# Kernel optimization log

Hardware: AMD Instinct MI355X
Metric: run time of the kernel (lower is better)

## Reference

```python
import jax, jax.numpy as jnp
import numpy as np
from functools import partial

# ---- constants mirroring init_kwargs ----
T, B, J, I = 1024, 32, 128, 512
KD = 16              # max_delay (dilated kernel size)
THETA = 1.0          # threshold
SIG = 0.5            # delay.SIG, frozen (requires_grad=False)
ALPHA = 5.0          # ATan surrogate alpha
EPS = 1e-5           # BatchNorm eps

# ---- ATan surrogate spike (spikingjelly): fwd = heaviside, bwd = atan grad ----
@jax.custom_vjp
def atan_spike(x):
    return (x >= 0).astype(x.dtype)

def _atan_fwd(x):
    return atan_spike(x), x

def _atan_bwd(x, g):
    return (g * (ALPHA / 2.0) / (1.0 + (jnp.pi / 2.0 * ALPHA * x) ** 2),)

atan_spike.defvjp(_atan_fwd, _atan_bwd)

def _dcls_kernel(w, P):
    # DCLS1d 'gauss' version, kernel_count=1: gaussian bump centered at P + KD//2,
    # normalized over the kernel axis, scaled by weight. w,P: (I,J) -> (I,J,KD)
    c = P + KD // 2
    k = jnp.arange(KD, dtype=w.dtype)                        # (KD,)
    g = jnp.exp(-0.5 * ((k[None, None, :] - c[:, :, None]) / SIG) ** 2)
    g = g / (g.sum(-1, keepdims=True) + 1e-7)
    return w[:, :, None] * g                                  # (I,J,KD)

def setup_inputs() -> dict:
    key = jax.random.key(0)
    ks = jax.random.split(key, 6)
    x = jax.random.normal(ks[0], (T, B, J), dtype=jnp.float32)
    # kaiming_uniform_ fan_in = J*1 -> bound = sqrt(6/fan_in)
    bound = float(np.sqrt(6.0 / J))
    delay_w = jax.random.uniform(ks[1], (I, J), jnp.float32, -bound, bound)
    # P ~ U(-max_delay//2, max_delay//2), then clamped (already in range)
    delay_P = jax.random.uniform(ks[2], (I, J), jnp.float32, -(KD // 2), KD // 2)
    beta = jax.random.uniform(ks[3], (I,), jnp.float32, 0.0, 1.0)
    bn_gamma = jnp.ones((I,), jnp.float32)
    bn_beta = jnp.zeros((I,), jnp.float32)
    U0 = jax.random.uniform(ks[4], (B, I), jnp.float32)       # RandomBatchwiseInit(0,1)
    return {"x": x, "delay_w": delay_w, "delay_P": delay_P, "beta": beta,
            "bn_gamma": bn_gamma, "bn_beta": bn_beta, "U0": U0}

def reference(x, delay_w, delay_P, beta, bn_gamma, bn_beta, U0):
    # --- delayed conv: (T,B,J) -> (B,J,T) -> left-pad KD-1 -> conv1d -> (T,B,I) ---
    xb = jnp.transpose(x, (1, 2, 0))                          # (B,J,T)
    xb = jnp.pad(xb, ((0, 0), (0, 0), (KD - 1, 0)))           # (B,J,T+KD-1)
    kern = _dcls_kernel(delay_w, delay_P)                     # (I,J,KD)
    y = jax.lax.conv_general_dilated(
        xb, kern, window_strides=(1,), padding='VALID',
        dimension_numbers=('NCH', 'OIH', 'NCH'))              # (B,I,T)
    y = jnp.transpose(y, (2, 0, 1))                           # (T,B,I)

    # --- BatchNorm1d over reshaped (T*B, I, 1): stats over T*B per channel ---
    yf = y.reshape(T * B, I)
    mean = yf.mean(axis=0)
    var = yf.var(axis=0)
    yf = (yf - mean) * jax.lax.rsqrt(var + EPS) * bn_gamma + bn_beta
    y = yf.reshape(T, B, I)

    # --- soft-reset LIF scan (NOTE: original passes RAW beta, not sigmoid(beta)) ---
    def step(carry, xt):
        Ut, St = carry
        Ut = beta * (Ut - THETA * St) + (1.0 - beta) * xt
        St = atan_spike(Ut - THETA)
        return (Ut, St), St

    S0 = jnp.zeros_like(U0)
    _, o = jax.lax.scan(step, (U0, S0), y)                    # (T,B,I)
    return o
```

## Files before the change

kernel.cpp:

```cpp
#include <hip/hip_runtime.h>

#define TT 1024
#define NB 32
#define NJ 128
#define NI 512
#define KD 16
#define LDP 40

typedef short bf16x8 __attribute__((ext_vector_type(8)));
typedef short bf16x4 __attribute__((ext_vector_type(4)));
typedef float floatx4 __attribute__((ext_vector_type(4)));

struct S3 { short h, m, l; };

__device__ __forceinline__ S3 split3(float v) {
    S3 o;
    unsigned hb = __float_as_uint(v) & 0xFFFF0000u;
    float hf = __uint_as_float(hb);
    float r1 = v - hf;
    unsigned mb = __float_as_uint(r1) & 0xFFFF0000u;
    float mf = __uint_as_float(mb);
    float r2 = r1 - mf;
    unsigned lb = __float_as_uint(r2) & 0xFFFF0000u;
    o.h = (short)(hb >> 16);
    o.m = (short)(mb >> 16);
    o.l = (short)(lb >> 16);
    return o;
}

__global__ __launch_bounds__(256) void dcls_kern(const float* __restrict__ w,
                                                 const float* __restrict__ P,
                                                 float* __restrict__ Wt) {
    int idx = blockIdx.x * 256 + threadIdx.x;
    int j = idx & (NJ - 1);
    int i = idx >> 7;
    float wv = w[i * NJ + j];
    float c  = P[i * NJ + j] + (float)(KD / 2);
    float g[KD];
    float s = 0.f;
#pragma unroll
    for (int k = 0; k < KD; ++k) {
        float u = (float)k - c;
        g[k] = expf(-2.0f * u * u);
        s += g[k];
    }
    float inv = wv / (s + 1e-7f);
#pragma unroll
    for (int k = 0; k < KD; ++k) {
        int d = (KD - 1) - k;
        Wt[(size_t)i * 2048 + d * NJ + j] = g[k] * inv;
    }
}

__global__ __launch_bounds__(256) void conv_mfma(const float* __restrict__ x,
                                                 const float* __restrict__ Wt,
                                                 float* __restrict__ y) {
    __shared__ short Ah[128][LDP];
    __shared__ short Am[128][LDP];
    __shared__ short Al[128][LDP];
    __shared__ short Wh[128][LDP];
    __shared__ short Wm[128][LDP];
    __shared__ short Wl[128][LDP];

    const int t0 = blockIdx.x * 128;
    const int i0 = blockIdx.y * 128;
    const int b  = blockIdx.z;
    const int tid = threadIdx.x;

    const int lane8 = tid & 7;
    const int rw    = tid >> 3;
    const int l    = tid & 63;
    const int wid  = tid >> 6;
    const int lr16 = l & 15;
    const int kb   = l >> 4;
    const int wm   = wid >> 1;
    const int wn   = wid & 1;

    floatx4 acc[4][4];
#pragma unroll
    for (int mf = 0; mf < 4; ++mf)
#pragma unroll
        for (int nf = 0; nf < 4; ++nf)
#pragma unroll
            for (int e = 0; e < 4; ++e) acc[mf][nf][e] = 0.f;

#pragma unroll 1
    for (int kk = 0; kk < 64; ++kk) {
        const int d   = kk >> 2;
        const int j0c = (kk & 3) << 5;

        float4 ga[4], gw[4];
#pragma unroll
        for (int s = 0; s < 4; ++s) {
            int r = rw + s * 32;
            int t = t0 + r - d;
            float4 va = make_float4(0.f, 0.f, 0.f, 0.f);
            if (t >= 0) va = *(const float4*)(x + ((size_t)t * NB + b) * NJ + j0c + lane8 * 4);
            ga[s] = va;
            gw[s] = *(const float4*)(Wt + (size_t)(i0 + r) * 2048 + kk * 32 + lane8 * 4);
        }

        __syncthreads();

#pragma unroll
        for (int s = 0; s < 4; ++s) {
            int r  = rw + s * 32;
            int c4 = lane8 * 4;
            S3 s0 = split3(ga[s].x), s1 = split3(ga[s].y), s2 = split3(ga[s].z), s3 = split3(ga[s].w);
            bf16x4 h4, m4, l4;
            h4[0] = s0.h; m4[0] = s0.m; l4[0] = s0.l;
            h4[1] = s1.h; m4[1] = s1.m; l4[1] = s1.l;
            h4[2] = s2.h; m4[2] = s2.m; l4[2] = s2.l;
            h4[3] = s3.h; m4[3] = s3.m; l4[3] = s3.l;
            *(bf16x4*)&Ah[r][c4] = h4;
            *(bf16x4*)&Am[r][c4] = m4;
            *(bf16x4*)&Al[r][c4] = l4;
            s0 = split3(gw[s].x); s1 = split3(gw[s].y); s2 = split3(gw[s].z); s3 = split3(gw[s].w);
            h4[0] = s0.h; m4[0] = s0.m; l4[0] = s0.l;
            h4[1] = s1.h; m4[1] = s1.m; l4[1] = s1.l;
            h4[2] = s2.h; m4[2] = s2.m; l4[2] = s2.l;
            h4[3] = s3.h; m4[3] = s3.m; l4[3] = s3.l;
            *(bf16x4*)&Wh[r][c4] = h4;
            *(bf16x4*)&Wm[r][c4] = m4;
            *(bf16x4*)&Wl[r][c4] = l4;
        }

        __syncthreads();

        bf16x8 bh[4], bm[4], bl2[4];
#pragma unroll
        for (int nf = 0; nf < 4; ++nf) {
            int row = wn * 64 + nf * 16 + lr16;
            bh[nf]  = *(const bf16x8*)&Wh[row][kb * 8];
            bm[nf]  = *(const bf16x8*)&Wm[row][kb * 8];
            bl2[nf] = *(const bf16x8*)&Wl[row][kb * 8];
        }
#pragma unroll
        for (int mf = 0; mf < 4; ++mf) {
            int row = wm * 64 + mf * 16 + lr16;
            bf16x8 ah = *(const bf16x8*)&Ah[row][kb * 8];
            bf16x8 am = *(const bf16x8*)&Am[row][kb * 8];
            bf16x8 al = *(const bf16x8*)&Al[row][kb * 8];
#pragma unroll
            for (int nf = 0; nf < 4; ++nf)
                acc[mf][nf] = __builtin_amdgcn_mfma_f32_16x16x32_bf16(ah, bh[nf], acc[mf][nf], 0, 0, 0);
#pragma unroll
            for (int nf = 0; nf < 4; ++nf)
                acc[mf][nf] = __builtin_amdgcn_mfma_f32_16x16x32_bf16(ah, bm[nf], acc[mf][nf], 0, 0, 0);
#pragma unroll
            for (int nf = 0; nf < 4; ++nf)
                acc[mf][nf] = __builtin_amdgcn_mfma_f32_16x16x32_bf16(am, bh[nf], acc[mf][nf], 0, 0, 0);
#pragma unroll
            for (int nf = 0; nf < 4; ++nf)
                acc[mf][nf] = __builtin_amdgcn_mfma_f32_16x16x32_bf16(am, bm[nf], acc[mf][nf], 0, 0, 0);
#pragma unroll
            for (int nf = 0; nf < 4; ++nf)
                acc[mf][nf] = __builtin_amdgcn_mfma_f32_16x16x32_bf16(ah, bl2[nf], acc[mf][nf], 0, 0, 0);
#pragma unroll
            for (int nf = 0; nf < 4; ++nf)
                acc[mf][nf] = __builtin_amdgcn_mfma_f32_16x16x32_bf16(al, bh[nf], acc[mf][nf], 0, 0, 0);
        }
    }

#pragma unroll
    for (int mf = 0; mf < 4; ++mf)
#pragma unroll
        for (int nf = 0; nf < 4; ++nf) {
            int ic = i0 + wn * 64 + nf * 16 + lr16;
#pragma unroll
            for (int q = 0; q < 4; ++q) {
                int t = t0 + wm * 64 + mf * 16 + kb * 4 + q;
                y[((size_t)t * NB + b) * NI + ic] = acc[mf][nf][q];
            }
        }
}

__global__ __launch_bounds__(256) void red1(const float* __restrict__ y,
                                            float* __restrict__ part) {
    int r0 = blockIdx.x * 128;
    int c  = threadIdx.x;
    float s0 = 0.f, q0 = 0.f, s1 = 0.f, q1 = 0.f;
#pragma unroll 4
    for (int r = 0; r < 128; ++r) {
        float v0 = y[(size_t)(r0 + r) * NI + c];
        float v1 = y[(size_t)(r0 + r) * NI + c + 256];
        s0 += v0; q0 = fmaf(v0, v0, q0);
        s1 += v1; q1 = fmaf(v1, v1, q1);
    }
    part[blockIdx.x * NI + c]            = s0;
    part[blockIdx.x * NI + c + 256]      = s1;
    part[256 * NI + blockIdx.x * NI + c]       = q0;
    part[256 * NI + blockIdx.x * NI + c + 256] = q1;
}

__global__ __launch_bounds__(512) void red2(const float* __restrict__ part,
                                            const float* __restrict__ gamma,
                                            const float* __restrict__ bbeta,
                                            float* __restrict__ sb) {
    int c = threadIdx.x;
    double s = 0.0, q = 0.0;
#pragma unroll 8
    for (int p = 0; p < 256; ++p) {
        s += (double)part[p * NI + c];
        q += (double)part[256 * NI + p * NI + c];
    }
    double mean = s / 32768.0;
    double var  = q / 32768.0 - mean * mean;
    double scale = (double)gamma[c] / sqrt(var + 1e-5);
    sb[c]      = (float)scale;
    sb[NI + c] = (float)((double)bbeta[c] - mean * scale);
}

__global__ __launch_bounds__(64) void scan_kern(float* __restrict__ y,
                                                const float* __restrict__ sb,
                                                const float* __restrict__ beta,
                                                const float* __restrict__ U0) {
    int g = blockIdx.x * 64 + threadIdx.x;
    int i = g & (NI - 1);
    float scale = sb[i];
    float bias  = sb[NI + i];
    float bet = beta[i];
    float omb = 1.f - bet;
    float u = U0[g];
    float s = 0.f;
    float* yp = y + g;

    float A[32], Bv[32];
#pragma unroll
    for (int r = 0; r < 32; ++r) A[r] = yp[(size_t)r * 16384];

    for (int t0 = 0; t0 < TT; t0 += 64) {
#pragma unroll
        for (int r = 0; r < 32; ++r) Bv[r] = yp[(size_t)(t0 + 32 + r) * 16384];
#pragma unroll
        for (int r = 0; r < 32; ++r) {
            float z = fmaf(A[r], scale, bias);
            u = fmaf(bet, u - s, omb * z);
            s = (u >= 1.f) ? 1.f : 0.f;
            yp[(size_t)(t0 + r) * 16384] = s;
        }
        if (t0 + 64 < TT) {
#pragma unroll
            for (int r = 0; r < 32; ++r) A[r] = yp[(size_t)(t0 + 64 + r) * 16384];
        }
#pragma unroll
        for (int r = 0; r < 32; ++r) {
            float z = fmaf(Bv[r], scale, bias);
            u = fmaf(bet, u - s, omb * z);
            s = (u >= 1.f) ? 1.f : 0.f;
            yp[(size_t)(t0 + 32 + r) * 16384] = s;
        }
    }
}

extern "C" void kernel_launch(void* const* d_in, const int* in_sizes, int n_in,
                              void* d_out, int out_size, void* d_ws, size_t ws_size,
                              hipStream_t stream) {
    const float* x       = (const float*)d_in[0];
    const float* delay_w = (const float*)d_in[1];
    const float* delay_P = (const float*)d_in[2];
    const float* beta    = (const float*)d_in[3];
    const float* bn_g    = (const float*)d_in[4];
    const float* bn_b    = (const float*)d_in[5];
    const float* U0      = (const float*)d_in[6];
    float* y = (float*)d_out;

    float* Wt   = (float*)d_ws;
    float* part = Wt + (size_t)NI * 2048;
    float* sb   = part + 2 * 256 * NI;

    dcls_kern<<<dim3(NI * NJ / 256), dim3(256), 0, stream>>>(delay_w, delay_P, Wt);
    conv_mfma<<<dim3(TT / 128, NI / 128, NB), dim3(256), 0, stream>>>(x, Wt, y);
    red1<<<dim3(TT * NB / 128), dim3(256), 0, stream>>>(y, part);
    red2<<<dim3(1), dim3(512), 0, stream>>>(part, bn_g, bn_b, sb);
    scan_kern<<<dim3(NB * NI / 64), dim3(64), 0, stream>>>(y, sb, beta, U0);
}
```

Baseline: 413.3 us.

## Prefetch next K-slice into registers and XOR-swizzle packed LDS tiles

Moves the global loads for the next K iteration after the second barrier, so they overlap with the MFMA work of the current iteration. Packs the hi/mid/lo bf16 splits into three 128x64 shared arrays, each row XOR-swizzled at 16-byte granularity, replacing the padded layout. Each thread now stores one 16-byte vector per split piece instead of 8-byte ones. Adds launch_bounds occupancy 3, which raises register pressure from holding the prefetched data across the MFMA section.

```diff
diff --git a/kernel.cpp b/kernel.cpp
--- a/kernel.cpp
+++ b/kernel.cpp
@@ -5,10 +5,8 @@
 #define NJ 128
 #define NI 512
 #define KD 16
-#define LDP 40
 
 typedef short bf16x8 __attribute__((ext_vector_type(8)));
-typedef short bf16x4 __attribute__((ext_vector_type(4)));
 typedef float floatx4 __attribute__((ext_vector_type(4)));
 
 struct S3 { short h, m, l; };
@@ -52,23 +50,20 @@
     }
 }
 
-__global__ __launch_bounds__(256) void conv_mfma(const float* __restrict__ x,
-                                                 const float* __restrict__ Wt,
-                                                 float* __restrict__ y) {
-    __shared__ short Ah[128][LDP];
-    __shared__ short Am[128][LDP];
-    __shared__ short Al[128][LDP];
-    __shared__ short Wh[128][LDP];
-    __shared__ short Wm[128][LDP];
-    __shared__ short Wl[128][LDP];
+__global__ __launch_bounds__(256, 3) void conv_mfma(const float* __restrict__ x,
+                                                    const float* __restrict__ Wt,
+                                                    float* __restrict__ y) {
+    __shared__ __align__(16) short PA[128][64];
+    __shared__ __align__(16) short PW[128][64];
+    __shared__ __align__(16) short PL[128][64];
 
     const int t0 = blockIdx.x * 128;
     const int i0 = blockIdx.y * 128;
     const int b  = blockIdx.z;
     const int tid = threadIdx.x;
 
-    const int lane8 = tid & 7;
-    const int rw    = tid >> 3;
+    const int ch   = tid & 3;
+    const int rw2  = tid >> 2;
     const int l    = tid & 63;
     const int wid  = tid >> 6;
     const int lr16 = l & 15;
@@ -84,63 +79,98 @@
 #pragma unroll
             for (int e = 0; e < 4; ++e) acc[mf][nf][e] = 0.f;
 
+    float4 ga[2][2], gw[2][2];
+#pragma unroll
+    for (int s = 0; s < 2; ++s) {
+        int r = rw2 + s * 64;
+        int t = t0 + r;
+        const float* ax = x + ((size_t)t * NB + b) * NJ + ch * 8;
+        ga[s][0] = *(const float4*)ax;
+        ga[s][1] = *(const float4*)(ax + 4);
+        const float* wp = Wt + (size_t)(i0 + r) * 2048 + ch * 8;
+        gw[s][0] = *(const float4*)wp;
+        gw[s][1] = *(const float4*)(wp + 4);
+    }
+
 #pragma unroll 1
     for (int kk = 0; kk < 64; ++kk) {
-        const int d   = kk >> 2;
-        const int j0c = (kk & 3) << 5;
-
-        float4 ga[4], gw[4];
-#pragma unroll
-        for (int s = 0; s < 4; ++s) {
-            int r = rw + s * 32;
-            int t = t0 + r - d;
-            float4 va = make_float4(0.f, 0.f, 0.f, 0.f);
-            if (t >= 0) va = *(const float4*)(x + ((size_t)t * NB + b) * NJ + j0c + lane8 * 4);
-            ga[s] = va;
-            gw[s] = *(const float4*)(Wt + (size_t)(i0 + r) * 2048 + kk * 32 + lane8 * 4);
-        }
-
         __syncthreads();
 
 #pragma unroll
-        for (int s = 0; s < 4; ++s) {
-            int r  = rw + s * 32;
-            int c4 = lane8 * 4;
-            S3 s0 = split3(ga[s].x), s1 = split3(ga[s].y), s2 = split3(ga[s].z), s3 = split3(ga[s].w);
-            bf16x4 h4, m4, l4;
-            h4[0] = s0.h; m4[0] = s0.m; l4[0] = s0.l;
-            h4[1] = s1.h; m4[1] = s1.m; l4[1] = s1.l;
-            h4[2] = s2.h; m4[2] = s2.m; l4[2] = s2.l;
-            h4[3] = s3.h; m4[3] = s3.m; l4[3] = s3.l;
-            *(bf16x4*)&Ah[r][c4] = h4;
-            *(bf16x4*)&Am[r][c4] = m4;
-            *(bf16x4*)&Al[r][c4] = l4;
-            s0 = split3(gw[s].x); s1 = split3(gw[s].y); s2 = split3(gw[s].z); s3 = split3(gw[s].w);
-            h4[0] = s0.h; m4[0] = s0.m; l4[0] = s0.l;
-            h4[1] = s1.h; m4[1] = s1.m; l4[1] = s1.l;
-            h4[2] = s2.h; m4[2] = s2.m; l4[2] = s2.l;
-            h4[3] = s3.h; m4[3] = s3.m; l4[3] = s3.l;
-            *(bf16x4*)&Wh[r][c4] = h4;
-            *(bf16x4*)&Wm[r][c4] = m4;
-            *(bf16x4*)&Wl[r][c4] = l4;
+        for (int s = 0; s < 2; ++s) {
+            int r   = rw2 + s * 64;
+            int key = r & 7;
+            char* rowA = (char*)PA + r * 128;
+            char* rowW = (char*)PW + r * 128;
+            char* rowL = (char*)PL + r * 128;
+            bf16x8 h8, m8, l8;
+#pragma unroll
+            for (int q = 0; q < 2; ++q) {
+                float4 v = ga[s][q];
+                S3 a = split3(v.x), bb = split3(v.y), cc = split3(v.z), dd = split3(v.w);
+                h8[q*4+0] = a.h;  h8[q*4+1] = bb.h; h8[q*4+2] = cc.h; h8[q*4+3] = dd.h;
+                m8[q*4+0] = a.m;  m8[q*4+1] = bb.m; m8[q*4+2] = cc.m; m8[q*4+3] = dd.m;
+                l8[q*4+0] = a.l;  l8[q*4+1] = bb.l; l8[q*4+2] = cc.l; l8[q*4+3] = dd.l;
+            }
+            *(bf16x8*)(rowA + ((ch     ^ key) * 16)) = h8;
+            *(bf16x8*)(rowA + (((ch+4) ^ key) * 16)) = m8;
+            *(bf16x8*)(rowL + ((ch     ^ key) * 16)) = l8;
+#pragma unroll
+            for (int q = 0; q < 2; ++q) {
+                float4 v = gw[s][q];
+                S3 a = split3(v.x), bb = split3(v.y), cc = split3(v.z), dd = split3(v.w);
+                h8[q*4+0] = a.h;  h8[q*4+1] = bb.h; h8[q*4+2] = cc.h; h8[q*4+3] = dd.h;
+                m8[q*4+0] = a.m;  m8[q*4+1] = bb.m; m8[q*4+2] = cc.m; m8[q*4+3] = dd.m;
+                l8[q*4+0] = a.l;  l8[q*4+1] = bb.l; l8[q*4+2] = cc.l; l8[q*4+3] = dd.l;
+            }
+            *(bf16x8*)(rowW + ((ch     ^ key) * 16)) = h8;
+            *(bf16x8*)(rowW + (((ch+4) ^ key) * 16)) = m8;
+            *(bf16x8*)(rowL + (((ch+4) ^ key) * 16)) = l8;
         }
 
         __syncthreads();
+
+        if (kk + 1 < 64) {
+            const int kn  = kk + 1;
+            const int d   = kn >> 2;
+            const int j0c = (kn & 3) << 5;
+#pragma unroll
+            for (int s = 0; s < 2; ++s) {
+                int r = rw2 + s * 64;
+                int t = t0 + r - d;
+                float4 z = make_float4(0.f, 0.f, 0.f, 0.f);
+                ga[s][0] = z; ga[s][1] = z;
+                if (t >= 0) {
+                    const float* ax = x + ((size_t)t * NB + b) * NJ + j0c + ch * 8;
+                    ga[s][0] = *(const float4*)ax;
+                    ga[s][1] = *(const float4*)(ax + 4);
+                }
+                const float* wp = Wt + (size_t)(i0 + r) * 2048 + kn * 32 + ch * 8;
+                gw[s][0] = *(const float4*)wp;
+                gw[s][1] = *(const float4*)(wp + 4);
+            }
+        }
 
         bf16x8 bh[4], bm[4], bl2[4];
 #pragma unroll
         for (int nf = 0; nf < 4; ++nf) {
             int row = wn * 64 + nf * 16 + lr16;
-            bh[nf]  = *(const bf16x8*)&Wh[row][kb * 8];
-            bm[nf]  = *(const bf16x8*)&Wm[row][kb * 8];
-            bl2[nf] = *(const bf16x8*)&Wl[row][kb * 8];
+            int key = row & 7;
+            const char* rowW = (const char*)PW + row * 128;
+            const char* rowL = (const char*)PL + row * 128;
+            bh[nf]  = *(const bf16x8*)(rowW + ((kb     ^ key) * 16));
+            bm[nf]  = *(const bf16x8*)(rowW + (((kb+4) ^ key) * 16));
+            bl2[nf] = *(const bf16x8*)(rowL + (((kb+4) ^ key) * 16));
         }
 #pragma unroll
         for (int mf = 0; mf < 4; ++mf) {
             int row = wm * 64 + mf * 16 + lr16;
-            bf16x8 ah = *(const bf16x8*)&Ah[row][kb * 8];
-            bf16x8 am = *(const bf16x8*)&Am[row][kb * 8];
-            bf16x8 al = *(const bf16x8*)&Al[row][kb * 8];
+            int key = row & 7;
+            const char* rowA = (const char*)PA + row * 128;
+            const char* rowL = (const char*)PL + row * 128;
+            bf16x8 ah = *(const bf16x8*)(rowA + ((kb     ^ key) * 16));
+            bf16x8 am = *(const bf16x8*)(rowA + (((kb+4) ^ key) * 16));
+            bf16x8 al = *(const bf16x8*)(rowL + ((kb     ^ key) * 16));
 #pragma unroll
             for (int nf = 0; nf < 4; ++nf)
                 acc[mf][nf] = __builtin_amdgcn_mfma_f32_16x16x32_bf16(ah, bh[nf], acc[mf][nf], 0, 0, 0);
```

New measurement: 436.2 us. +5.5%, slower.

## Pre-split weights into MFMA fragment layout and read them directly from global

Applied to the files above, without the earlier changes.

The DCLS kernel now writes the weights already split into three bf16 levels and stored in MFMA fragment order, so the conv kernel loads B fragments straight from global memory instead of staging them through shared memory and splitting them on every tile. The A tile is packed into swizzled shared memory (hi and mid in one array, lo in another) to avoid bank conflicts. The next step's x and weights are prefetched into registers while the current step runs its MFMAs, and launch bounds ask for two blocks per CU. This saves shared-memory traffic and repeated split work, at the cost of more register pressure and workspace aliasing: WF and the reduction partials share the same workspace region, which is safe only because the conv kernel finishes before red1 starts.

```diff
diff --git a/kernel.cpp b/kernel.cpp
--- a/kernel.cpp
+++ b/kernel.cpp
@@ -5,10 +5,9 @@
 #define NJ 128
 #define NI 512
 #define KD 16
-#define LDP 40
+#define LVL 1048576
 
 typedef short bf16x8 __attribute__((ext_vector_type(8)));
-typedef short bf16x4 __attribute__((ext_vector_type(4)));
 typedef float floatx4 __attribute__((ext_vector_type(4)));
 
 struct S3 { short h, m, l; };
@@ -30,7 +29,7 @@
 
 __global__ __launch_bounds__(256) void dcls_kern(const float* __restrict__ w,
                                                  const float* __restrict__ P,
-                                                 float* __restrict__ Wt) {
+                                                 short* __restrict__ WF) {
     int idx = blockIdx.x * 256 + threadIdx.x;
     int j = idx & (NJ - 1);
     int i = idx >> 7;
@@ -45,30 +44,30 @@
         s += g[k];
     }
     float inv = wv / (s + 1e-7f);
-#pragma unroll
-    for (int k = 0; k < KD; ++k) {
-        int d = (KD - 1) - k;
-        Wt[(size_t)i * 2048 + d * NJ + j] = g[k] * inv;
-    }
-}
-
-__global__ __launch_bounds__(256) void conv_mfma(const float* __restrict__ x,
-                                                 const float* __restrict__ Wt,
-                                                 float* __restrict__ y) {
-    __shared__ short Ah[128][LDP];
-    __shared__ short Am[128][LDP];
-    __shared__ short Al[128][LDP];
-    __shared__ short Wh[128][LDP];
-    __shared__ short Wm[128][LDP];
-    __shared__ short Wl[128][LDP];
+    size_t base = (size_t)(i >> 4) * 32768 + (size_t)(j >> 3) * 128 + (i & 15) * 8 + (j & 7);
+#pragma unroll
+    for (int d = 0; d < KD; ++d) {
+        S3 sp = split3(g[(KD - 1) - d] * inv);
+        size_t off = base + (size_t)d * 2048;
+        WF[off]           = sp.h;
+        WF[off + LVL]     = sp.m;
+        WF[off + 2 * LVL] = sp.l;
+    }
+}
+
+__global__ __launch_bounds__(256, 2) void conv_mfma(const float* __restrict__ x,
+                                                    const short* __restrict__ WF,
+                                                    float* __restrict__ y) {
+    __shared__ __align__(16) short PA[128][64];
+    __shared__ __align__(16) short PL[128][64];
 
     const int t0 = blockIdx.x * 128;
     const int i0 = blockIdx.y * 128;
     const int b  = blockIdx.z;
     const int tid = threadIdx.x;
 
-    const int lane8 = tid & 7;
-    const int rw    = tid >> 3;
+    const int ch   = tid & 3;
+    const int rw2  = tid >> 2;
     const int l    = tid & 63;
     const int wid  = tid >> 6;
     const int lr16 = l & 15;
@@ -76,6 +75,13 @@
     const int wm   = wid >> 1;
     const int wn   = wid & 1;
 
+    const short* pnf[4];
+#pragma unroll
+    for (int nf = 0; nf < 4; ++nf) {
+        int ig = (i0 + wn * 64 + nf * 16) >> 4;
+        pnf[nf] = WF + (size_t)ig * 32768 + l * 8;
+    }
+
     floatx4 acc[4][4];
 #pragma unroll
     for (int mf = 0; mf < 4; ++mf)
@@ -84,83 +90,90 @@
 #pragma unroll
             for (int e = 0; e < 4; ++e) acc[mf][nf][e] = 0.f;
 
+    float4 ga[2][2];
+    bf16x8 W0h[4], W0m[4], W0l[4], W1h[4], W1m[4], W1l[4];
+
+#define LOADW(K, H, M, L_) {                                                    \
+    int koff = ((((K) >> 2) * 16 + ((K) & 3) * 4)) * 128;                       \
+    _Pragma("unroll") for (int nf = 0; nf < 4; ++nf) {                          \
+        const short* p = pnf[nf] + koff;                                        \
+        H[nf]  = *(const bf16x8*)(p);                                           \
+        M[nf]  = *(const bf16x8*)(p + LVL);                                     \
+        L_[nf] = *(const bf16x8*)(p + 2 * LVL); } }
+
+#define STEP(K, CH, CM, CL, NH, NM, NL) {                                       \
+    __syncthreads();                                                            \
+    _Pragma("unroll") for (int s = 0; s < 2; ++s) {                             \
+        int r = rw2 + s * 64;                                                   \
+        int key = r & 7;                                                        \
+        char* rowA = (char*)PA + r * 128;                                       \
+        char* rowL = (char*)PL + r * 128;                                       \
+        S3 a0 = split3(ga[s][0].x), a1 = split3(ga[s][0].y),                    \
+           a2 = split3(ga[s][0].z), a3 = split3(ga[s][0].w),                    \
+           a4 = split3(ga[s][1].x), a5 = split3(ga[s][1].y),                    \
+           a6 = split3(ga[s][1].z), a7 = split3(ga[s][1].w);                    \
+        bf16x8 h8, m8, l8;                                                      \
+        h8[0]=a0.h; h8[1]=a1.h; h8[2]=a2.h; h8[3]=a3.h;                         \
+        h8[4]=a4.h; h8[5]=a5.h; h8[6]=a6.h; h8[7]=a7.h;                         \
+        m8[0]=a0.m; m8[1]=a1.m; m8[2]=a2.m; m8[3]=a3.m;                         \
+        m8[4]=a4.m; m8[5]=a5.m; m8[6]=a6.m; m8[7]=a7.m;                         \
+        l8[0]=a0.l; l8[1]=a1.l; l8[2]=a2.l; l8[3]=a3.l;                         \
+        l8[4]=a4.l; l8[5]=a5.l; l8[6]=a6.l; l8[7]=a7.l;                         \
+        *(bf16x8*)(rowA + ((ch ^ key) * 16))       = h8;                        \
+        *(bf16x8*)(rowA + (((ch + 4) ^ key) * 16)) = m8;                        \
+        *(bf16x8*)(rowL + ((ch ^ key) * 16))       = l8; }                      \
+    __syncthreads();                                                            \
+    if ((K) + 1 < 64) {                                                         \
+        int kn = (K) + 1, dn = kn >> 2, j0n = (kn & 3) << 5;                    \
+        _Pragma("unroll") for (int s = 0; s < 2; ++s) {                         \
+            int r = rw2 + s * 64;                                               \
+            int t = t0 + r - dn;                                                \
+            float4 z4 = make_float4(0.f, 0.f, 0.f, 0.f);                        \
+            ga[s][0] = z4; ga[s][1] = z4;                                       \
+            if (t >= 0) {                                                       \
+                const float* ax = x + ((size_t)t * NB + b) * NJ + j0n + ch * 8; \
+                ga[s][0] = *(const float4*)ax;                                  \
+                ga[s][1] = *(const float4*)(ax + 4); } }                        \
+        LOADW(kn, NH, NM, NL) }                                                 \
+    _Pragma("unroll") for (int mf = 0; mf < 4; ++mf) {                          \
+        int row = wm * 64 + mf * 16 + lr16;                                     \
+        int key = row & 7;                                                      \
+        const char* rowA = (const char*)PA + row * 128;                         \
+        const char* rowL = (const char*)PL + row * 128;                         \
+        bf16x8 ah = *(const bf16x8*)(rowA + ((kb ^ key) * 16));                 \
+        bf16x8 am = *(const bf16x8*)(rowA + (((kb + 4) ^ key) * 16));           \
+        bf16x8 al = *(const bf16x8*)(rowL + ((kb ^ key) * 16));                 \
+        _Pragma("unroll") for (int nf = 0; nf < 4; ++nf)                        \
+            acc[mf][nf] = __builtin_amdgcn_mfma_f32_16x16x32_bf16(ah, CH[nf], acc[mf][nf], 0, 0, 0); \
+        _Pragma("unroll") for (int nf = 0; nf < 4; ++nf)                        \
+            acc[mf][nf] = __builtin_amdgcn_mfma_f32_16x16x32_bf16(ah, CM[nf], acc[mf][nf], 0, 0, 0); \
+        _Pragma("unroll") for (int nf = 0; nf < 4; ++nf)                        \
+            acc[mf][nf] = __builtin_amdgcn_mfma_f32_16x16x32_bf16(am, CH[nf], acc[mf][nf], 0, 0, 0); \
+        _Pragma("unroll") for (int nf = 0; nf < 4; ++nf)                        \
+            acc[mf][nf] = __builtin_amdgcn_mfma_f32_16x16x32_bf16(am, CM[nf], acc[mf][nf], 0, 0, 0); \
+        _Pragma("unroll") for (int nf = 0; nf < 4; ++nf)                        \
+            acc[mf][nf] = __builtin_amdgcn_mfma_f32_16x16x32_bf16(ah, CL[nf], acc[mf][nf], 0, 0, 0); \
+        _Pragma("unroll") for (int nf = 0; nf < 4; ++nf)                        \
+            acc[mf][nf] = __builtin_amdgcn_mfma_f32_16x16x32_bf16(al, CH[nf], acc[mf][nf], 0, 0, 0); \
+    } }
+
+#pragma unroll
+    for (int s = 0; s < 2; ++s) {
+        int r = rw2 + s * 64;
+        int t = t0 + r;
+        const float* ax = x + ((size_t)t * NB + b) * NJ + ch * 8;
+        ga[s][0] = *(const float4*)ax;
+        ga[s][1] = *(const float4*)(ax + 4);
+    }
+    LOADW(0, W0h, W0m, W0l)
+
 #pragma unroll 1
-    for (int kk = 0; kk < 64; ++kk) {
-        const int d   = kk >> 2;
-        const int j0c = (kk & 3) << 5;
-
-        float4 ga[4], gw[4];
-#pragma unroll
-        for (int s = 0; s < 4; ++s) {
-            int r = rw + s * 32;
-            int t = t0 + r - d;
-            float4 va = make_float4(0.f, 0.f, 0.f, 0.f);
-            if (t >= 0) va = *(const float4*)(x + ((size_t)t * NB + b) * NJ + j0c + lane8 * 4);
-            ga[s] = va;
-            gw[s] = *(const float4*)(Wt + (size_t)(i0 + r) * 2048 + kk * 32 + lane8 * 4);
-        }
-
-        __syncthreads();
-
-#pragma unroll
-        for (int s = 0; s < 4; ++s) {
-            int r  = rw + s * 32;
-            int c4 = lane8 * 4;
-            S3 s0 = split3(ga[s].x), s1 = split3(ga[s].y), s2 = split3(ga[s].z), s3 = split3(ga[s].w);
-            bf16x4 h4, m4, l4;
-            h4[0] = s0.h; m4[0] = s0.m; l4[0] = s0.l;
-            h4[1] = s1.h; m4[1] = s1.m; l4[1] = s1.l;
-            h4[2] = s2.h; m4[2] = s2.m; l4[2] = s2.l;
-            h4[3] = s3.h; m4[3] = s3.m; l4[3] = s3.l;
-            *(bf16x4*)&Ah[r][c4] = h4;
-            *(bf16x4*)&Am[r][c4] = m4;
-            *(bf16x4*)&Al[r][c4] = l4;
-            s0 = split3(gw[s].x); s1 = split3(gw[s].y); s2 = split3(gw[s].z); s3 = split3(gw[s].w);
-            h4[0] = s0.h; m4[0] = s0.m; l4[0] = s0.l;
-            h4[1] = s1.h; m4[1] = s1.m; l4[1] = s1.l;
-            h4[2] = s2.h; m4[2] = s2.m; l4[2] = s2.l;
-            h4[3] = s3.h; m4[3] = s3.m; l4[3] = s3.l;
-            *(bf16x4*)&Wh[r][c4] = h4;
-            *(bf16x4*)&Wm[r][c4] = m4;
-            *(bf16x4*)&Wl[r][c4] = l4;
-        }
-
-        __syncthreads();
-
-        bf16x8 bh[4], bm[4], bl2[4];
-#pragma unroll
-        for (int nf = 0; nf < 4; ++nf) {
-            int row = wn * 64 + nf * 16 + lr16;
-            bh[nf]  = *(const bf16x8*)&Wh[row][kb * 8];
-            bm[nf]  = *(const bf16x8*)&Wm[row][kb * 8];
-            bl2[nf] = *(const bf16x8*)&Wl[row][kb * 8];
-        }
-#pragma unroll
-        for (int mf = 0; mf < 4; ++mf) {
-            int row = wm * 64 + mf * 16 + lr16;
-            bf16x8 ah = *(const bf16x8*)&Ah[row][kb * 8];
-            bf16x8 am = *(const bf16x8*)&Am[row][kb * 8];
-            bf16x8 al = *(const bf16x8*)&Al[row][kb * 8];
-#pragma unroll
-            for (int nf = 0; nf < 4; ++nf)
-                acc[mf][nf] = __builtin_amdgcn_mfma_f32_16x16x32_bf16(ah, bh[nf], acc[mf][nf], 0, 0, 0);
-#pragma unroll
-            for (int nf = 0; nf < 4; ++nf)
-                acc[mf][nf] = __builtin_amdgcn_mfma_f32_16x16x32_bf16(ah, bm[nf], acc[mf][nf], 0, 0, 0);
-#pragma unroll
-            for (int nf = 0; nf < 4; ++nf)
-                acc[mf][nf] = __builtin_amdgcn_mfma_f32_16x16x32_bf16(am, bh[nf], acc[mf][nf], 0, 0, 0);
-#pragma unroll
-            for (int nf = 0; nf < 4; ++nf)
-                acc[mf][nf] = __builtin_amdgcn_mfma_f32_16x16x32_bf16(am, bm[nf], acc[mf][nf], 0, 0, 0);
-#pragma unroll
-            for (int nf = 0; nf < 4; ++nf)
-                acc[mf][nf] = __builtin_amdgcn_mfma_f32_16x16x32_bf16(ah, bl2[nf], acc[mf][nf], 0, 0, 0);
-#pragma unroll
-            for (int nf = 0; nf < 4; ++nf)
-                acc[mf][nf] = __builtin_amdgcn_mfma_f32_16x16x32_bf16(al, bh[nf], acc[mf][nf], 0, 0, 0);
-        }
-    }
+    for (int kk = 0; kk < 64; kk += 2) {
+        STEP(kk,     W0h, W0m, W0l, W1h, W1m, W1l)
+        STEP(kk + 1, W1h, W1m, W1l, W0h, W0m, W0l)
+    }
+#undef LOADW
+#undef STEP
 
 #pragma unroll
     for (int mf = 0; mf < 4; ++mf)
@@ -265,12 +278,12 @@
     const float* U0      = (const float*)d_in[6];
     float* y = (float*)d_out;
 
-    float* Wt   = (float*)d_ws;
-    float* part = Wt + (size_t)NI * 2048;
-    float* sb   = part + 2 * 256 * NI;
-
-    dcls_kern<<<dim3(NI * NJ / 256), dim3(256), 0, stream>>>(delay_w, delay_P, Wt);
-    conv_mfma<<<dim3(TT / 128, NI / 128, NB), dim3(256), 0, stream>>>(x, Wt, y);
+    short* WF   = (short*)d_ws;
+    float* part = (float*)d_ws;
+    float* sb   = (float*)d_ws + 2 * 256 * NI;
+
+    dcls_kern<<<dim3(NI * NJ / 256), dim3(256), 0, stream>>>(delay_w, delay_P, WF);
+    conv_mfma<<<dim3(TT / 128, NI / 128, NB), dim3(256), 0, stream>>>(x, WF, y);
     red1<<<dim3(TT * NB / 128), dim3(256), 0, stream>>>(y, part);
     red2<<<dim3(1), dim3(512), 0, stream>>>(part, bn_g, bn_b, sb);
     scan_kern<<<dim3(NB * NI / 64), dim3(64), 0, stream>>>(y, sb, beta, U0);
```

New measurement: 367.8 us. -11.0%, faster.
